# Performance work log

Hardware: AMD Instinct MI355X
Metric: run time of the kernel (lower is better)

Reference implementation:

```python
import jax, jax.numpy as jnp
import numpy as np

N = 100000  # nodes
E = 800000  # edges (before self-loops)
D = 64      # in_dim == out_dim


def setup_inputs() -> dict:
    key = jax.random.key(0)
    k_x, k_e, k_w, k_b = jax.random.split(key, 4)
    x = jax.random.normal(k_x, (N, D), dtype=jnp.float32)
    edge_index = jax.random.randint(k_e, (2, E), 0, N, dtype=jnp.int64)
    # GCNConv linear params (PyG: glorot weight, zero bias; random here)
    W = jax.random.normal(k_w, (D, D), dtype=jnp.float32) / np.sqrt(D)
    b = jax.random.normal(k_b, (D,), dtype=jnp.float32) * 0.01
    return {"x": x, "W": W, "b": b, "edge_index": edge_index}


def reference(x, W, b, edge_index):
    n = x.shape[0]
    # GCNConv: linear transform first
    h = x @ W.T  # [N, D]
    # add self-loops (PyG default add_self_loops=True)
    loops = jnp.arange(n, dtype=edge_index.dtype)
    src = jnp.concatenate([edge_index[0], loops])
    dst = jnp.concatenate([edge_index[1], loops])
    # symmetric normalization D^{-1/2} A D^{-1/2} (degrees include self-loops)
    deg = jax.ops.segment_sum(jnp.ones_like(dst, dtype=h.dtype), dst, num_segments=n)
    dinv = jnp.where(deg > 0, jax.lax.rsqrt(deg), 0.0)
    norm = dinv[src] * dinv[dst]  # [E+N]
    # gather -> scale -> scatter-add
    msg = h[src] * norm[:, None]  # [E+N, D]
    agg = jax.ops.segment_sum(msg, dst, num_segments=n) + b  # [N, D]
    # residual (in_dim == out_dim -> identity residual) + ReLU
    return jax.nn.relu(agg + x)
```

## Files before the change

### kernel.cpp

```cpp
#include <hip/hip_runtime.h>


#define NN 100000
#define NE 800000
#define DD 64
#define CAP 32
#define ECHUNK 4096
#define NBLK 196
#define NG 512
#define RCAP 40
#define GN 196
#define BMAX 2048

typedef unsigned int uint;
typedef unsigned short ushort;
typedef __attribute__((ext_vector_type(8))) short short8v;
typedef __attribute__((ext_vector_type(4))) float f32x4v;

__device__ __forceinline__ ushort f2bf(float f) {
    uint u = __float_as_uint(f);
    u += 0x7fffu + ((u >> 16) & 1u);
    return (ushort)(u >> 16);
}
__device__ __forceinline__ float bflo(uint u) { return __uint_as_float(u << 16); }
__device__ __forceinline__ float bfhi(uint u) { return __uint_as_float(u & 0xffff0000u); }

__global__ __launch_bounds__(256) void route_kernel(const int* __restrict__ ei,
                                                    int2* __restrict__ route,
                                                    int* __restrict__ counts) {
    __shared__ int lcnt[NG];
    int t = threadIdx.x;
    for (int m = t; m < NG; m += 256) lcnt[m] = 0;
    __syncthreads();

    int blk = blockIdx.x;
#pragma unroll
    for (int p = 0; p < 4; ++p) {
        int base = blk * ECHUNK + p * 1024 + t * 4;
        if (base < NE) {
            int4 sv = *(const int4*)(ei + base);
            int4 dv = *(const int4*)(ei + NE + base);
            int s[4] = {sv.x, sv.y, sv.z, sv.w};
            int d[4] = {dv.x, dv.y, dv.z, dv.w};
#pragma unroll
            for (int j = 0; j < 4; ++j) {
                int g = d[j] & (NG - 1);
                int rk = atomicAdd(&lcnt[g], 1);
                if (rk < RCAP)
                    route[(size_t)(blk * NG + g) * RCAP + rk] =
                        make_int2(s[j], d[j]);
            }
        }
    }
    __syncthreads();
    for (int m = t; m < NG; m += 256) counts[blk * NG + m] = lcnt[m];
}

__global__ __launch_bounds__(256) void place_kernel(const int2* __restrict__ route,
                                                    const int* __restrict__ counts,
                                                    int* __restrict__ cur,
                                                    int* __restrict__ srcIdx) {
    __shared__ int    pref[256];
    __shared__ int    base_s[256];
    __shared__ int    cnt_s[GN];
    __shared__ ushort blkmap[BMAX];

    int g = blockIdx.x;
    int t = threadIdx.x;

    int c = 0;
    if (t < NBLK) {
        c = counts[t * NG + g];
        if (c > RCAP) c = RCAP;
    }
    pref[t] = c;
    __syncthreads();
#pragma unroll
    for (int off = 1; off < 256; off <<= 1) {
        int v = (t >= off) ? pref[t - off] : 0;
        __syncthreads();
        pref[t] += v;
        __syncthreads();
    }
    base_s[t] = pref[t] - c;
    for (int m = t; m < GN; m += 256) cnt_s[m] = 0;
    __syncthreads();

    int total = pref[255];
    if (total > BMAX) total = BMAX;

    if (t < NBLK) {
        int beg = base_s[t];
        for (int i = 0; i < c; ++i) {
            int idx = beg + i;
            if (idx < BMAX) blkmap[idx] = (ushort)t;
        }
    }
    __syncthreads();

    for (int j = t; j < total; j += 256) {
        int blk = blkmap[j];
        int2 e = route[(size_t)(blk * NG + g) * RCAP + (j - base_s[blk])];
        int m = e.y >> 9;
        int cc = atomicAdd(&cnt_s[m], 1);
        if (cc < CAP) srcIdx[(e.y << 5) + cc] = e.x;
    }
    __syncthreads();

    for (int m = t; m * NG + g < NN; m += 256)
        cur[m * NG + g] = cnt_s[m];
}

__global__ __launch_bounds__(256) void fill_kernel(const int* __restrict__ ei,
                                                   int* __restrict__ cur,
                                                   int* __restrict__ srcIdx) {
    int base = (blockIdx.x * 256 + threadIdx.x) * 4;
    if (base >= NE) return;
    int4 sv = *(const int4*)(ei + base);
    int4 dv = *(const int4*)(ei + NE + base);
    int c0 = atomicAdd(&cur[dv.x], 1);
    int c1 = atomicAdd(&cur[dv.y], 1);
    int c2 = atomicAdd(&cur[dv.z], 1);
    int c3 = atomicAdd(&cur[dv.w], 1);
    if (c0 < CAP) srcIdx[(dv.x << 5) + c0] = sv.x;
    if (c1 < CAP) srcIdx[(dv.y << 5) + c1] = sv.y;
    if (c2 < CAP) srcIdx[(dv.z << 5) + c2] = sv.z;
    if (c3 < CAP) srcIdx[(dv.w << 5) + c3] = sv.w;
}

__global__ __launch_bounds__(256) void linear_kernel(const float* __restrict__ x,
                                                     const float* __restrict__ W,
                                                     const int* __restrict__ deg,
                                                     ushort* __restrict__ hq) {
    int wave = (blockIdx.x * 256 + threadIdx.x) >> 6;
    int lane = threadIdx.x & 63;
    if (wave >= NN / 16) return;
    int rowBase = wave * 16;
    int r16 = lane & 15;
    int lg  = lane >> 4;

    short8v bfr[4][2];
#pragma unroll
    for (int ct = 0; ct < 4; ++ct)
#pragma unroll
        for (int kb = 0; kb < 2; ++kb) {
            const float* wp = W + (ct * 16 + r16) * 64 + kb * 32 + lg * 8;
            float4 w0 = *(const float4*)(wp);
            float4 w1 = *(const float4*)(wp + 4);
            short8v tv;
            tv[0] = (short)f2bf(w0.x); tv[1] = (short)f2bf(w0.y);
            tv[2] = (short)f2bf(w0.z); tv[3] = (short)f2bf(w0.w);
            tv[4] = (short)f2bf(w1.x); tv[5] = (short)f2bf(w1.y);
            tv[6] = (short)f2bf(w1.z); tv[7] = (short)f2bf(w1.w);
            bfr[ct][kb] = tv;
        }

    short8v af[2];
#pragma unroll
    for (int kb = 0; kb < 2; ++kb) {
        const float* xp = x + (size_t)(rowBase + r16) * 64 + kb * 32 + lg * 8;
        float4 a0 = *(const float4*)(xp);
        float4 a1 = *(const float4*)(xp + 4);
        short8v tv;
        tv[0] = (short)f2bf(a0.x); tv[1] = (short)f2bf(a0.y);
        tv[2] = (short)f2bf(a0.z); tv[3] = (short)f2bf(a0.w);
        tv[4] = (short)f2bf(a1.x); tv[5] = (short)f2bf(a1.y);
        tv[6] = (short)f2bf(a1.z); tv[7] = (short)f2bf(a1.w);
        af[kb] = tv;
    }

    f32x4v acc[4];
#pragma unroll
    for (int ct = 0; ct < 4; ++ct) {
        acc[ct] = (f32x4v){0.f, 0.f, 0.f, 0.f};
        acc[ct] = __builtin_amdgcn_mfma_f32_16x16x32_bf16(af[0], bfr[ct][0],
                                                          acc[ct], 0, 0, 0);
        acc[ct] = __builtin_amdgcn_mfma_f32_16x16x32_bf16(af[1], bfr[ct][1],
                                                          acc[ct], 0, 0, 0);
    }

    float sc[4];
#pragma unroll
    for (int r = 0; r < 4; ++r)
        sc[r] = rsqrtf((float)deg[rowBase + lg * 4 + r] + 1.0f);
#pragma unroll
    for (int ct = 0; ct < 4; ++ct)
#pragma unroll
        for (int r = 0; r < 4; ++r)
            hq[(size_t)(rowBase + lg * 4 + r) * 64 + ct * 16 + r16] =
                f2bf(acc[ct][r] * sc[r]);
}

__global__ __launch_bounds__(256) void gather_kernel(const int* __restrict__ srcIdx,
                                                     const int* __restrict__ deg,
                                                     const uint4* __restrict__ hq4,
                                                     const float4* __restrict__ x4,
                                                     const float* __restrict__ b,
                                                     float4* __restrict__ out4) {
    int t = blockIdx.x * blockDim.x + threadIdx.x;
    int node = t >> 3;
    int l = t & 7;
    if (node >= NN) return;

    int dg = deg[node];
    float di = rsqrtf((float)dg + 1.0f);
    if (dg > CAP) dg = CAP;

    uint4 vs = hq4[(size_t)node * 8 + l];
    int4  u  = ((const int4*)srcIdx)[node * 8 + l];
    float4 xa = x4[(size_t)node * 16 + l * 2];
    float4 xb = x4[(size_t)node * 16 + l * 2 + 1];

    float acc[8];
    acc[0] = bflo(vs.x); acc[1] = bfhi(vs.x);
    acc[2] = bflo(vs.y); acc[3] = bfhi(vs.y);
    acc[4] = bflo(vs.z); acc[5] = bfhi(vs.z);
    acc[6] = bflo(vs.w); acc[7] = bfhi(vs.w);

    int base = (threadIdx.x & 63) & ~7;

#define ACC8(v)                                        \
    acc[0] += bflo((v).x); acc[1] += bfhi((v).x);      \
    acc[2] += bflo((v).y); acc[3] += bfhi((v).y);      \
    acc[4] += bflo((v).z); acc[5] += bfhi((v).z);      \
    acc[6] += bflo((v).w); acc[7] += bfhi((v).w);

#define GROUP(GI)                                                              \
    {                                                                          \
        int la = base + 2 * (GI), lb = la + 1, eb = (GI) * 8;                  \
        int s0 = __shfl(u.x, la, 64), s1 = __shfl(u.y, la, 64);                \
        int s2 = __shfl(u.z, la, 64), s3 = __shfl(u.w, la, 64);                \
        int s4 = __shfl(u.x, lb, 64), s5 = __shfl(u.y, lb, 64);                \
        int s6 = __shfl(u.z, lb, 64), s7 = __shfl(u.w, lb, 64);                \
        uint4 z = make_uint4(0u, 0u, 0u, 0u);                                  \
        uint4 v0 = z, v1 = z, v2 = z, v3 = z, v4 = z, v5 = z, v6 = z, v7 = z;  \
        if (eb + 0 < dg) v0 = hq4[(size_t)s0 * 8 + l];                         \
        if (eb + 1 < dg) v1 = hq4[(size_t)s1 * 8 + l];                         \
        if (eb + 2 < dg) v2 = hq4[(size_t)s2 * 8 + l];                         \
        if (eb + 3 < dg) v3 = hq4[(size_t)s3 * 8 + l];                         \
        if (eb + 4 < dg) v4 = hq4[(size_t)s4 * 8 + l];                         \
        if (eb + 5 < dg) v5 = hq4[(size_t)s5 * 8 + l];                         \
        if (eb + 6 < dg) v6 = hq4[(size_t)s6 * 8 + l];                         \
        if (eb + 7 < dg) v7 = hq4[(size_t)s7 * 8 + l];                         \
        ACC8(v0); ACC8(v1); ACC8(v2); ACC8(v3);                                \
        ACC8(v4); ACC8(v5); ACC8(v6); ACC8(v7);                                \
    }

    GROUP(0)
    if (dg > 8)  GROUP(1)
    if (dg > 16) GROUP(2)
    if (dg > 24) GROUP(3)

#undef GROUP
#undef ACC8

    float4 oa, ob;
    int cb = l * 8;
    oa.x = fmaxf(di * acc[0] + b[cb + 0] + xa.x, 0.f);
    oa.y = fmaxf(di * acc[1] + b[cb + 1] + xa.y, 0.f);
    oa.z = fmaxf(di * acc[2] + b[cb + 2] + xa.z, 0.f);
    oa.w = fmaxf(di * acc[3] + b[cb + 3] + xa.w, 0.f);
    ob.x = fmaxf(di * acc[4] + b[cb + 4] + xb.x, 0.f);
    ob.y = fmaxf(di * acc[5] + b[cb + 5] + xb.y, 0.f);
    ob.z = fmaxf(di * acc[6] + b[cb + 6] + xb.z, 0.f);
    ob.w = fmaxf(di * acc[7] + b[cb + 7] + xb.w, 0.f);
    out4[(size_t)node * 16 + l * 2]     = oa;
    out4[(size_t)node * 16 + l * 2 + 1] = ob;
}

extern "C" void kernel_launch(void* const* d_in, const int* in_sizes, int n_in,
                              void* d_out, int out_size, void* d_ws, size_t ws_size,
                              hipStream_t stream) {
    const float* x = (const float*)d_in[0];
    const float* W = (const float*)d_in[1];
    const float* b = (const float*)d_in[2];
    const int* ei = (const int*)d_in[3];

    char* ws = (char*)d_ws;
    int*    cur    = (int*)(ws + 0);
    int*    srcIdx = (int*)(ws + 400000);
    ushort* hq     = (ushort*)(ws + 13200000);
    int2*   route  = (int2*)(ws + 26000000);
    int*    counts = (int*)(ws + 58112640);
    const size_t WS_NEED = 58514048;

    if (ws_size >= WS_NEED) {
        route_kernel<<<NBLK, 256, 0, stream>>>(ei, route, counts);
        place_kernel<<<NG, 256, 0, stream>>>(route, counts, cur, srcIdx);
    } else {
        hipMemsetAsync(cur, 0, NN * sizeof(int), stream);
        fill_kernel<<<(NE / 4 + 255) / 256, 256, 0, stream>>>(ei, cur, srcIdx);
    }
    linear_kernel<<<(NN / 16 + 3) / 4, 256, 0, stream>>>(x, W, cur, hq);
    gather_kernel<<<NN / 32, 256, 0, stream>>>(srcIdx, cur, (const uint4*)hq,
                                               (const float4*)x, b, (float4*)d_out);
}
```

Baseline: 137.2 us.

## Fuse linear transform with edge routing and move source-degree scaling into gather

The linear kernel no longer scales rows by the source degree, so it no longer depends on the degree counts. That lets it run in the same launch as the routing kernel, with extra blocks branching on block index. The gather kernel now looks up each neighbor's degree, computes its rsqrt and broadcasts the weights by shuffle, scaling each gathered row. This removes one kernel launch and the serial dependency, at the cost of extra random degree reads and multiplies in the gather.

Measured after the change: 138.5 us. No clear change (+0.9%).

```diff
diff --git a/kernel.cpp b/kernel.cpp
--- a/kernel.cpp
+++ b/kernel.cpp
@@ -11,6 +11,7 @@
 #define RCAP 40
 #define GN 196
 #define BMAX 2048
+#define NLIN 1563
 
 typedef unsigned int uint;
 typedef unsigned short ushort;
@@ -25,15 +26,12 @@
 __device__ __forceinline__ float bflo(uint u) { return __uint_as_float(u << 16); }
 __device__ __forceinline__ float bfhi(uint u) { return __uint_as_float(u & 0xffff0000u); }
 
-__global__ __launch_bounds__(256) void route_kernel(const int* __restrict__ ei,
-                                                    int2* __restrict__ route,
-                                                    int* __restrict__ counts) {
-    __shared__ int lcnt[NG];
-    int t = threadIdx.x;
+__device__ __forceinline__ void route_body(int blk, int t, int* lcnt,
+                                           const int* __restrict__ ei,
+                                           int2* __restrict__ route,
+                                           int* __restrict__ counts) {
     for (int m = t; m < NG; m += 256) lcnt[m] = 0;
     __syncthreads();
-
-    int blk = blockIdx.x;
 #pragma unroll
     for (int p = 0; p < 4; ++p) {
         int base = blk * ECHUNK + p * 1024 + t * 4;
@@ -54,6 +52,82 @@
     }
     __syncthreads();
     for (int m = t; m < NG; m += 256) counts[blk * NG + m] = lcnt[m];
+}
+
+__device__ __forceinline__ void linear_body(int lb, int t,
+                                            const float* __restrict__ x,
+                                            const float* __restrict__ W,
+                                            ushort* __restrict__ hq) {
+    int wave = (lb * 256 + t) >> 6;
+    int lane = t & 63;
+    if (wave >= NN / 16) return;
+    int rowBase = wave * 16;
+    int r16 = lane & 15;
+    int lg  = lane >> 4;
+
+    short8v bfr[4][2];
+#pragma unroll
+    for (int ct = 0; ct < 4; ++ct)
+#pragma unroll
+        for (int kb = 0; kb < 2; ++kb) {
+            const float* wp = W + (ct * 16 + r16) * 64 + kb * 32 + lg * 8;
+            float4 w0 = *(const float4*)(wp);
+            float4 w1 = *(const float4*)(wp + 4);
+            short8v tv;
+            tv[0] = (short)f2bf(w0.x); tv[1] = (short)f2bf(w0.y);
+            tv[2] = (short)f2bf(w0.z); tv[3] = (short)f2bf(w0.w);
+            tv[4] = (short)f2bf(w1.x); tv[5] = (short)f2bf(w1.y);
+            tv[6] = (short)f2bf(w1.z); tv[7] = (short)f2bf(w1.w);
+            bfr[ct][kb] = tv;
+        }
+
+    short8v af[2];
+#pragma unroll
+    for (int kb = 0; kb < 2; ++kb) {
+        const float* xp = x + (size_t)(rowBase + r16) * 64 + kb * 32 + lg * 8;
+        float4 a0 = *(const float4*)(xp);
+        float4 a1 = *(const float4*)(xp + 4);
+        short8v tv;
+        tv[0] = (short)f2bf(a0.x); tv[1] = (short)f2bf(a0.y);
+        tv[2] = (short)f2bf(a0.z); tv[3] = (short)f2bf(a0.w);
+        tv[4] = (short)f2bf(a1.x); tv[5] = (short)f2bf(a1.y);
+        tv[6] = (short)f2bf(a1.z); tv[7] = (short)f2bf(a1.w);
+        af[kb] = tv;
+    }
+
+    f32x4v acc[4];
+#pragma unroll
+    for (int ct = 0; ct < 4; ++ct) {
+        acc[ct] = (f32x4v){0.f, 0.f, 0.f, 0.f};
+        acc[ct] = __builtin_amdgcn_mfma_f32_16x16x32_bf16(af[0], bfr[ct][0],
+                                                          acc[ct], 0, 0, 0);
+        acc[ct] = __builtin_amdgcn_mfma_f32_16x16x32_bf16(af[1], bfr[ct][1],
+                                                          acc[ct], 0, 0, 0);
+    }
+
+#pragma unroll
+    for (int ct = 0; ct < 4; ++ct)
+#pragma unroll
+        for (int r = 0; r < 4; ++r)
+            hq[(size_t)(rowBase + lg * 4 + r) * 64 + ct * 16 + r16] =
+                f2bf(acc[ct][r]);
+}
+
+__global__ __launch_bounds__(256) void fused_route_linear(
+        const int* __restrict__ ei, int2* __restrict__ route,
+        int* __restrict__ counts, const float* __restrict__ x,
+        const float* __restrict__ W, ushort* __restrict__ hq) {
+    __shared__ int lcnt[NG];
+    if (blockIdx.x < NBLK)
+        route_body(blockIdx.x, threadIdx.x, lcnt, ei, route, counts);
+    else
+        linear_body(blockIdx.x - NBLK, threadIdx.x, x, W, hq);
+}
+
+__global__ __launch_bounds__(256) void linear_kernel(const float* __restrict__ x,
+                                                     const float* __restrict__ W,
+                                                     ushort* __restrict__ hq) {
+    linear_body(blockIdx.x, threadIdx.x, x, W, hq);
 }
 
 __global__ __launch_bounds__(256) void place_kernel(const int2* __restrict__ route,
@@ -128,69 +202,6 @@
     if (c3 < CAP) srcIdx[(dv.w << 5) + c3] = sv.w;
 }
 
-__global__ __launch_bounds__(256) void linear_kernel(const float* __restrict__ x,
-                                                     const float* __restrict__ W,
-                                                     const int* __restrict__ deg,
-                                                     ushort* __restrict__ hq) {
-    int wave = (blockIdx.x * 256 + threadIdx.x) >> 6;
-    int lane = threadIdx.x & 63;
-    if (wave >= NN / 16) return;
-    int rowBase = wave * 16;
-    int r16 = lane & 15;
-    int lg  = lane >> 4;
-
-    short8v bfr[4][2];
-#pragma unroll
-    for (int ct = 0; ct < 4; ++ct)
-#pragma unroll
-        for (int kb = 0; kb < 2; ++kb) {
-            const float* wp = W + (ct * 16 + r16) * 64 + kb * 32 + lg * 8;
-            float4 w0 = *(const float4*)(wp);
-            float4 w1 = *(const float4*)(wp + 4);
-            short8v tv;
-            tv[0] = (short)f2bf(w0.x); tv[1] = (short)f2bf(w0.y);
-            tv[2] = (short)f2bf(w0.z); tv[3] = (short)f2bf(w0.w);
-            tv[4] = (short)f2bf(w1.x); tv[5] = (short)f2bf(w1.y);
-            tv[6] = (short)f2bf(w1.z); tv[7] = (short)f2bf(w1.w);
-            bfr[ct][kb] = tv;
-        }
-
-    short8v af[2];
-#pragma unroll
-    for (int kb = 0; kb < 2; ++kb) {
-        const float* xp = x + (size_t)(rowBase + r16) * 64 + kb * 32 + lg * 8;
-        float4 a0 = *(const float4*)(xp);
-        float4 a1 = *(const float4*)(xp + 4);
-        short8v tv;
-        tv[0] = (short)f2bf(a0.x); tv[1] = (short)f2bf(a0.y);
-        tv[2] = (short)f2bf(a0.z); tv[3] = (short)f2bf(a0.w);
-        tv[4] = (short)f2bf(a1.x); tv[5] = (short)f2bf(a1.y);
-        tv[6] = (short)f2bf(a1.z); tv[7] = (short)f2bf(a1.w);
-        af[kb] = tv;
-    }
-
-    f32x4v acc[4];
-#pragma unroll
-    for (int ct = 0; ct < 4; ++ct) {
-        acc[ct] = (f32x4v){0.f, 0.f, 0.f, 0.f};
-        acc[ct] = __builtin_amdgcn_mfma_f32_16x16x32_bf16(af[0], bfr[ct][0],
-                                                          acc[ct], 0, 0, 0);
-        acc[ct] = __builtin_amdgcn_mfma_f32_16x16x32_bf16(af[1], bfr[ct][1],
-                                                          acc[ct], 0, 0, 0);
-    }
-
-    float sc[4];
-#pragma unroll
-    for (int r = 0; r < 4; ++r)
-        sc[r] = rsqrtf((float)deg[rowBase + lg * 4 + r] + 1.0f);
-#pragma unroll
-    for (int ct = 0; ct < 4; ++ct)
-#pragma unroll
-        for (int r = 0; r < 4; ++r)
-            hq[(size_t)(rowBase + lg * 4 + r) * 64 + ct * 16 + r16] =
-                f2bf(acc[ct][r] * sc[r]);
-}
-
 __global__ __launch_bounds__(256) void gather_kernel(const int* __restrict__ srcIdx,
                                                      const int* __restrict__ deg,
                                                      const uint4* __restrict__ hq4,
@@ -211,19 +222,25 @@
     float4 xa = x4[(size_t)node * 16 + l * 2];
     float4 xb = x4[(size_t)node * 16 + l * 2 + 1];
 
+    int sb = l * 4;
+    float w0l = (sb + 0 < dg) ? rsqrtf((float)deg[u.x] + 1.0f) : 0.f;
+    float w1l = (sb + 1 < dg) ? rsqrtf((float)deg[u.y] + 1.0f) : 0.f;
+    float w2l = (sb + 2 < dg) ? rsqrtf((float)deg[u.z] + 1.0f) : 0.f;
+    float w3l = (sb + 3 < dg) ? rsqrtf((float)deg[u.w] + 1.0f) : 0.f;
+
     float acc[8];
-    acc[0] = bflo(vs.x); acc[1] = bfhi(vs.x);
-    acc[2] = bflo(vs.y); acc[3] = bfhi(vs.y);
-    acc[4] = bflo(vs.z); acc[5] = bfhi(vs.z);
-    acc[6] = bflo(vs.w); acc[7] = bfhi(vs.w);
+    acc[0] = di * bflo(vs.x); acc[1] = di * bfhi(vs.x);
+    acc[2] = di * bflo(vs.y); acc[3] = di * bfhi(vs.y);
+    acc[4] = di * bflo(vs.z); acc[5] = di * bfhi(vs.z);
+    acc[6] = di * bflo(vs.w); acc[7] = di * bfhi(vs.w);
 
     int base = (threadIdx.x & 63) & ~7;
 
-#define ACC8(v)                                        \
-    acc[0] += bflo((v).x); acc[1] += bfhi((v).x);      \
-    acc[2] += bflo((v).y); acc[3] += bfhi((v).y);      \
-    acc[4] += bflo((v).z); acc[5] += bfhi((v).z);      \
-    acc[6] += bflo((v).w); acc[7] += bfhi((v).w);
+#define ACC8(v, e)                                                 \
+    acc[0] += (e) * bflo((v).x); acc[1] += (e) * bfhi((v).x);      \
+    acc[2] += (e) * bflo((v).y); acc[3] += (e) * bfhi((v).y);      \
+    acc[4] += (e) * bflo((v).z); acc[5] += (e) * bfhi((v).z);      \
+    acc[6] += (e) * bflo((v).w); acc[7] += (e) * bfhi((v).w);
 
 #define GROUP(GI)                                                              \
     {                                                                          \
@@ -232,6 +249,10 @@
         int s2 = __shfl(u.z, la, 64), s3 = __shfl(u.w, la, 64);                \
         int s4 = __shfl(u.x, lb, 64), s5 = __shfl(u.y, lb, 64);                \
         int s6 = __shfl(u.z, lb, 64), s7 = __shfl(u.w, lb, 64);                \
+        float e0 = __shfl(w0l, la, 64), e1 = __shfl(w1l, la, 64);              \
+        float e2 = __shfl(w2l, la, 64), e3 = __shfl(w3l, la, 64);              \
+        float e4 = __shfl(w0l, lb, 64), e5 = __shfl(w1l, lb, 64);              \
+        float e6 = __shfl(w2l, lb, 64), e7 = __shfl(w3l, lb, 64);              \
         uint4 z = make_uint4(0u, 0u, 0u, 0u);                                  \
         uint4 v0 = z, v1 = z, v2 = z, v3 = z, v4 = z, v5 = z, v6 = z, v7 = z;  \
         if (eb + 0 < dg) v0 = hq4[(size_t)s0 * 8 + l];                         \
@@ -242,8 +263,8 @@
         if (eb + 5 < dg) v5 = hq4[(size_t)s5 * 8 + l];                         \
         if (eb + 6 < dg) v6 = hq4[(size_t)s6 * 8 + l];                         \
         if (eb + 7 < dg) v7 = hq4[(size_t)s7 * 8 + l];                         \
-        ACC8(v0); ACC8(v1); ACC8(v2); ACC8(v3);                                \
-        ACC8(v4); ACC8(v5); ACC8(v6); ACC8(v7);                                \
+        ACC8(v0, e0); ACC8(v1, e1); ACC8(v2, e2); ACC8(v3, e3);                \
+        ACC8(v4, e4); ACC8(v5, e5); ACC8(v6, e6); ACC8(v7, e7);                \
     }
 
     GROUP(0)
@@ -285,13 +306,14 @@
     const size_t WS_NEED = 58514048;
 
     if (ws_size >= WS_NEED) {
-        route_kernel<<<NBLK, 256, 0, stream>>>(ei, route, counts);
+        fused_route_linear<<<NBLK + NLIN, 256, 0, stream>>>(ei, route, counts,
+                                                            x, W, hq);
         place_kernel<<<NG, 256, 0, stream>>>(route, counts, cur, srcIdx);
     } else {
         hipMemsetAsync(cur, 0, NN * sizeof(int), stream);
         fill_kernel<<<(NE / 4 + 255) / 256, 256, 0, stream>>>(ei, cur, srcIdx);
-    }
-    linear_kernel<<<(NN / 16 + 3) / 4, 256, 0, stream>>>(x, W, cur, hq);
+        linear_kernel<<<NLIN, 256, 0, stream>>>(x, W, hq);
+    }
     gather_kernel<<<NN / 32, 256, 0, stream>>>(srcIdx, cur, (const uint4*)hq,
                                                (const float4*)x, b, (float4*)d_out);
 }
```
